# Kernel optimization log

Measured on AMD Instinct MI355X. Metric: run time of the kernel, lower is better.

## Reference

```python
import jax, jax.numpy as jnp
import numpy as np

INPUT_SIZE = 84 * 84 * 4  # 28224
FEATURE_SIZE = 1500
BATCH = 256

def setup_inputs() -> dict:
    key = jax.random.key(0)
    k_x, k_we, k_wd = jax.random.split(key, 3)
    scale_e = 1.0 / np.sqrt(INPUT_SIZE)
    scale_d = 1.0 / np.sqrt(FEATURE_SIZE)
    return {
        "x": jax.random.normal(k_x, (BATCH, INPUT_SIZE), dtype=jnp.float32),
        "W_enc": jax.random.normal(k_we, (FEATURE_SIZE, INPUT_SIZE), dtype=jnp.float32) * scale_e,
        "b_enc": jnp.zeros((FEATURE_SIZE,), dtype=jnp.float32),
        "W_dec": jax.random.normal(k_wd, (INPUT_SIZE, FEATURE_SIZE), dtype=jnp.float32) * scale_d,
        "b_dec": jnp.zeros((INPUT_SIZE,), dtype=jnp.float32),
    }

def reference(x, W_enc, b_enc, W_dec, b_dec):
    # Encoder: y_enc = sigmoid(x @ W_enc^T + b_enc), shape [B, F]
    y_enc = jax.nn.sigmoid(jnp.einsum('bi,fi->bf', x, W_enc) + b_enc)
    # Contractive (Jacobian Frobenius norm) term, closed form:
    # d y_enc[b,i] / d x[b,:] = y*(1-y) * W_enc[i,:]
    # jac_reg = sum_{b,i} (y*(1-y))^2 * ||W_enc[i,:]||^2
    s2 = jnp.square(y_enc * (1.0 - y_enc))          # [B, F]
    row_norm2 = jnp.sum(jnp.square(W_enc), axis=1)  # [F]
    jac_reg = jnp.sum(s2 * row_norm2)               # scalar
    # Decoder
    y_out = jax.nn.sigmoid(jnp.einsum('bf,if->bi', y_enc, W_dec) + b_dec)
    return y_out, jac_reg
```

## Files before the change

### kernel.cpp

```cpp
#include <hip/hip_runtime.h>
#include <hip/hip_bf16.h>


#define BATCH 256
#define IN    28224
#define FEAT  1500
#define FPAD  1536
#define KPAD  1504
#define ENC_S 21

typedef __attribute__((ext_vector_type(8))) short short8;
typedef __attribute__((ext_vector_type(4))) float f32x4;

__device__ __forceinline__ unsigned pack2(float lo, float hi) {
    unsigned a = __float_as_uint(lo) + 0x8000u;
    unsigned b = __float_as_uint(hi) + 0x8000u;
    return __builtin_amdgcn_perm(b, a, 0x07060302);
}
__device__ __forceinline__ unsigned short f2bf(float f) {
    unsigned u = __float_as_uint(f);
    return (unsigned short)((u + 0x7FFFu + ((u >> 16) & 1u)) >> 16);
}

__device__ __forceinline__ void async16(const unsigned short* g, unsigned short* l) {
    __builtin_amdgcn_global_load_lds(
        (const __attribute__((address_space(1))) unsigned int*)g,
        (__attribute__((address_space(3))) unsigned int*)l,
        16, 0, 0);
}


__global__ __launch_bounds__(256) void cvt_x(const float* __restrict__ x,
                                             unsigned short* __restrict__ xbf) {
    int idx = blockIdx.x * 256 + threadIdx.x;
    float4 v = ((const float4*)x)[idx];
    ((uint2*)xbf)[idx] = make_uint2(pack2(v.x, v.y), pack2(v.z, v.w));
}

__global__ __launch_bounds__(256) void wcvt_enc(const float* __restrict__ We,
                                                unsigned short* __restrict__ Webf,
                                                float* __restrict__ rn2) {
    const int row = blockIdx.y;
    const int t = threadIdx.x;
    const float4* src = (const float4*)(We + (long)row * IN) + blockIdx.x * 1008;
    uint2* dst = (uint2*)(Webf + (long)row * IN) + blockIdx.x * 1008;
    float sq = 0.f;
#pragma unroll
    for (int j = 0; j < 4; ++j) {
        int i = j * 256 + t;
        if (i < 1008) {
            float4 v = src[i];
            dst[i] = make_uint2(pack2(v.x, v.y), pack2(v.z, v.w));
            sq += v.x*v.x + v.y*v.y + v.z*v.z + v.w*v.w;
        }
    }
#pragma unroll
    for (int off = 32; off > 0; off >>= 1) sq += __shfl_down(sq, off);
    __shared__ float red[4];
    if ((t & 63) == 0) red[t >> 6] = sq;
    __syncthreads();
    if (t == 0) atomicAdd(&rn2[row], red[0] + red[1] + red[2] + red[3]);
}

__global__ __launch_bounds__(256) void wcvt_dec(const float* __restrict__ Wd,
                                                unsigned short* __restrict__ Wdbf) {
    int i = blockIdx.x * 256 + threadIdx.x;
    if (i >= 10584000) return;
    unsigned row = (unsigned)i / 375u;
    unsigned c   = (unsigned)i - row * 375u;
    float4 v = ((const float4*)Wd)[i];
    uint2* dst = (uint2*)Wdbf + (long)row * 376 + c;
    *dst = make_uint2(pack2(v.x, v.y), pack2(v.z, v.w));
    if (c == 374) dst[1] = make_uint2(0u, 0u);
}


__global__ __launch_bounds__(256) void enc_gemm_f(const unsigned short* __restrict__ xbf,
                                                  const unsigned short* __restrict__ Webf,
                                                  float* __restrict__ part) {
    __shared__ unsigned short As[128 * 32];
    __shared__ unsigned short Bs[64 * 32];

    const int m0 = (blockIdx.x & 1) * 128;
    const int n0 = (blockIdx.x >> 1) * 64;
    const int kb = blockIdx.y * 1344;
    const int t    = threadIdx.x;
    const int lane = t & 63;
    const int w    = t >> 6;
    const int l15  = lane & 15;
    const int quad = lane >> 4;
    const int wm   = w & 1;
    const int wn   = w >> 1;

    const unsigned short* ga0 = xbf + (long)(m0 + w * 32 + (lane >> 2)) * IN + kb + (lane & 3) * 8;
    const unsigned short* ga1 = ga0 + (long)16 * IN;
    const unsigned short* gb  = Webf + (long)(n0 + w * 16 + (lane >> 2)) * IN + kb + (lane & 3) * 8;
    unsigned short* la0 = As + (w * 32) * 32;
    unsigned short* la1 = As + (w * 32 + 16) * 32;
    unsigned short* lb  = Bs + (w * 16) * 32;

    f32x4 acc[4][2];
#pragma unroll
    for (int mt = 0; mt < 4; ++mt)
#pragma unroll
        for (int nt = 0; nt < 2; ++nt) { f32x4 z = {0.f,0.f,0.f,0.f}; acc[mt][nt] = z; }

    for (int k = 0; k < 1344; k += 32) {
        __syncthreads();
        async16(ga0 + k, la0);
        async16(ga1 + k, la1);
        async16(gb  + k, lb);
        __syncthreads();

        short8 a[4], b[2];
#pragma unroll
        for (int mt = 0; mt < 4; ++mt)
            a[mt] = *(const short8*)(As + (wm * 64 + mt * 16 + l15) * 32 + quad * 8);
#pragma unroll
        for (int nt = 0; nt < 2; ++nt)
            b[nt] = *(const short8*)(Bs + (wn * 32 + nt * 16 + l15) * 32 + quad * 8);
#pragma unroll
        for (int mt = 0; mt < 4; ++mt)
#pragma unroll
            for (int nt = 0; nt < 2; ++nt)
                acc[mt][nt] = __builtin_amdgcn_mfma_f32_16x16x32_bf16(a[mt], b[nt], acc[mt][nt], 0, 0, 0);
    }

    float* ps = part + (long)blockIdx.y * (BATCH * FPAD);
#pragma unroll
    for (int nt = 0; nt < 2; ++nt) {
        const int col = n0 + wn * 32 + nt * 16 + l15;
#pragma unroll
        for (int mt = 0; mt < 4; ++mt) {
            const int row = m0 + wm * 64 + mt * 16 + quad * 4;
#pragma unroll
            for (int r = 0; r < 4; ++r)
                ps[(long)(row + r) * FPAD + col] = acc[mt][nt][r];
        }
    }
}

__global__ __launch_bounds__(256) void act_jac_f(const float* __restrict__ part,
                                                 const float* __restrict__ be,
                                                 const float* __restrict__ rn2,
                                                 unsigned short* __restrict__ yenc,
                                                 float* __restrict__ jac) {
    const int b = blockIdx.y;
    const int f = blockIdx.x * 256 + threadIdx.x;
    float local = 0.0f;
    unsigned short h = 0;
    if (f < FEAT) {
        float p = be[f];
#pragma unroll 3
        for (int s = 0; s < ENC_S; ++s)
            p += part[(long)(s * BATCH + b) * FPAD + f];
        float y = 1.0f / (1.0f + __expf(-p));
        h = f2bf(y);
        float sg = y * (1.0f - y);
        local = sg * sg * rn2[f];
    }
    if (f < KPAD) yenc[b * KPAD + f] = h;

    float v = local;
#pragma unroll
    for (int off = 32; off > 0; off >>= 1) v += __shfl_down(v, off);
    __shared__ float red[4];
    if ((threadIdx.x & 63) == 0) red[threadIdx.x >> 6] = v;
    __syncthreads();
    if (threadIdx.x == 0) atomicAdd(jac, red[0] + red[1] + red[2] + red[3]);
}

__global__ __launch_bounds__(256) void dec_gemm_f(const unsigned short* __restrict__ yenc,
                                                  const unsigned short* __restrict__ Wdbf,
                                                  const float* __restrict__ bd,
                                                  float* __restrict__ out) {
    __shared__ unsigned short As[128 * 32];
    __shared__ unsigned short Bs[64 * 32];

    const int m0 = (blockIdx.x & 1) * 128;
    const int n0 = (blockIdx.x >> 1) * 64;
    const int t    = threadIdx.x;
    const int lane = t & 63;
    const int w    = t >> 6;
    const int l15  = lane & 15;
    const int quad = lane >> 4;
    const int wm   = w & 1;
    const int wn   = w >> 1;

    const unsigned short* ga0 = yenc + (long)(m0 + w * 32 + (lane >> 2)) * KPAD + (lane & 3) * 8;
    const unsigned short* ga1 = ga0 + (long)16 * KPAD;
    const unsigned short* gb  = Wdbf + (long)(n0 + w * 16 + (lane >> 2)) * KPAD + (lane & 3) * 8;
    unsigned short* la0 = As + (w * 32) * 32;
    unsigned short* la1 = As + (w * 32 + 16) * 32;
    unsigned short* lb  = Bs + (w * 16) * 32;

    f32x4 acc[4][2];
#pragma unroll
    for (int mt = 0; mt < 4; ++mt)
#pragma unroll
        for (int nt = 0; nt < 2; ++nt) { f32x4 z = {0.f,0.f,0.f,0.f}; acc[mt][nt] = z; }

    for (int k = 0; k < KPAD; k += 32) {
        __syncthreads();
        async16(ga0 + k, la0);
        async16(ga1 + k, la1);
        async16(gb  + k, lb);
        __syncthreads();

        short8 a[4], b[2];
#pragma unroll
        for (int mt = 0; mt < 4; ++mt)
            a[mt] = *(const short8*)(As + (wm * 64 + mt * 16 + l15) * 32 + quad * 8);
#pragma unroll
        for (int nt = 0; nt < 2; ++nt)
            b[nt] = *(const short8*)(Bs + (wn * 32 + nt * 16 + l15) * 32 + quad * 8);
#pragma unroll
        for (int mt = 0; mt < 4; ++mt)
#pragma unroll
            for (int nt = 0; nt < 2; ++nt)
                acc[mt][nt] = __builtin_amdgcn_mfma_f32_16x16x32_bf16(a[mt], b[nt], acc[mt][nt], 0, 0, 0);
    }

#pragma unroll
    for (int nt = 0; nt < 2; ++nt) {
        const int col = n0 + wn * 32 + nt * 16 + l15;
        const float bias = bd[col];
#pragma unroll
        for (int mt = 0; mt < 4; ++mt) {
            const int row = m0 + wm * 64 + mt * 16 + quad * 4;
#pragma unroll
            for (int r = 0; r < 4; ++r) {
                float v = acc[mt][nt][r] + bias;
                out[(long)(row + r) * IN + col] = 1.0f / (1.0f + __expf(-v));
            }
        }
    }
}

#define LDA 40

__global__ __launch_bounds__(256) void enc_gemm(const unsigned short* __restrict__ xbf,
                                                const float* __restrict__ We,
                                                float* __restrict__ preact,
                                                float* __restrict__ rn2) {
    __shared__ unsigned short As[256 * LDA];
    __shared__ unsigned short Bs[64 * LDA];
    const int n0 = blockIdx.x * 64;
    const int kb = blockIdx.y * 672;
    const int t = threadIdx.x, lane = t & 63, w = t >> 6, l15 = lane & 15, quad = lane >> 4;
    const unsigned short* asrc = xbf + (long)(t >> 2) * IN + (t & 3) * 8 + kb;
    unsigned short* adst = As + (t >> 2) * LDA + (t & 3) * 8;
    const int brow = t >> 3, bc4 = t & 7;
    const int f0 = n0 + brow, f1 = f0 + 32;
    const float* bsrc0 = We + (long)(f0 < FEAT ? f0 : FEAT - 1) * IN + bc4 * 4 + kb;
    const float* bsrc1 = We + (long)(f1 < FEAT ? f1 : FEAT - 1) * IN + bc4 * 4 + kb;
    unsigned short* bdst0 = Bs + brow * LDA + bc4 * 4;
    unsigned short* bdst1 = bdst0 + 32 * LDA;
    float rsq0 = 0.f, rsq1 = 0.f;
    f32x4 acc[4][4];
#pragma unroll
    for (int mt = 0; mt < 4; ++mt)
#pragma unroll
        for (int nt = 0; nt < 4; ++nt) { f32x4 z = {0.f,0.f,0.f,0.f}; acc[mt][nt] = z; }
    for (int k = 0; k < 672; k += 32) {
        short8 av[4];
#pragma unroll
        for (int j = 0; j < 4; ++j) av[j] = *(const short8*)(asrc + (long)64 * j * IN + k);
        const float4 bv0 = *(const float4*)(bsrc0 + k);
        const float4 bv1 = *(const float4*)(bsrc1 + k);
        __syncthreads();
#pragma unroll
        for (int j = 0; j < 4; ++j) *(short8*)(adst + 64 * j * LDA) = av[j];
        *(uint2*)bdst0 = make_uint2(pack2(bv0.x, bv0.y), pack2(bv0.z, bv0.w));
        *(uint2*)bdst1 = make_uint2(pack2(bv1.x, bv1.y), pack2(bv1.z, bv1.w));
        rsq0 += bv0.x*bv0.x + bv0.y*bv0.y + bv0.z*bv0.z + bv0.w*bv0.w;
        rsq1 += bv1.x*bv1.x + bv1.y*bv1.y + bv1.z*bv1.z + bv1.w*bv1.w;
        __syncthreads();
        short8 a[4], b[4];
#pragma unroll
        for (int mt = 0; mt < 4; ++mt) a[mt] = *(const short8*)(As + (w * 64 + mt * 16 + l15) * LDA + quad * 8);
#pragma unroll
        for (int nt = 0; nt < 4; ++nt) b[nt] = *(const short8*)(Bs + (nt * 16 + l15) * LDA + quad * 8);
#pragma unroll
        for (int mt = 0; mt < 4; ++mt)
#pragma unroll
            for (int nt = 0; nt < 4; ++nt)
                acc[mt][nt] = __builtin_amdgcn_mfma_f32_16x16x32_bf16(a[mt], b[nt], acc[mt][nt], 0, 0, 0);
    }
#pragma unroll
    for (int nt = 0; nt < 4; ++nt) {
        const int col = n0 + nt * 16 + l15;
        if (col < FEAT) {
#pragma unroll
            for (int mt = 0; mt < 4; ++mt) {
                float* p = preact + (long)(w * 64 + mt * 16 + quad * 4) * FEAT + col;
#pragma unroll
                for (int r = 0; r < 4; ++r) atomicAdd(p + (long)r * FEAT, acc[mt][nt][r]);
            }
        }
    }
    {
        float v0 = rsq0, v1 = rsq1;
#pragma unroll
        for (int off = 1; off < 8; off <<= 1) { v0 += __shfl_xor(v0, off); v1 += __shfl_xor(v1, off); }
        if ((lane & 7) == 0) {
            if (f0 < FEAT) atomicAdd(&rn2[f0], v0);
            if (f1 < FEAT) atomicAdd(&rn2[f1], v1);
        }
    }
}

__global__ __launch_bounds__(256) void act_jac(const float* __restrict__ preact,
                                               const float* __restrict__ be,
                                               const float* __restrict__ rn2,
                                               unsigned short* __restrict__ yenc,
                                               float* __restrict__ jac) {
    const int b = blockIdx.y;
    const int f = blockIdx.x * 256 + threadIdx.x;
    float local = 0.0f;
    unsigned short h = 0;
    if (f < FEAT) {
        float p = preact[b * FEAT + f] + be[f];
        float y = 1.0f / (1.0f + __expf(-p));
        h = f2bf(y);
        float s = y * (1.0f - y);
        local = s * s * rn2[f];
    }
    yenc[b * FPAD + f] = h;
    float v = local;
#pragma unroll
    for (int off = 32; off > 0; off >>= 1) v += __shfl_down(v, off);
    __shared__ float red[4];
    if ((threadIdx.x & 63) == 0) red[threadIdx.x >> 6] = v;
    __syncthreads();
    if (threadIdx.x == 0) atomicAdd(jac, red[0] + red[1] + red[2] + red[3]);
}

__global__ __launch_bounds__(256) void dec_gemm(const unsigned short* __restrict__ yenc,
                                                const float* __restrict__ Wd,
                                                const float* __restrict__ bd,
                                                float* __restrict__ out) {
    __shared__ unsigned short As[128 * LDA];
    __shared__ unsigned short Bs[64 * LDA];
    const int m0 = (blockIdx.x & 1) * 128;
    const int n0 = (blockIdx.x >> 1) * 64;
    const int t = threadIdx.x, lane = t & 63, w = t >> 6, l15 = lane & 15, quad = lane >> 4;
    const int mrow = (w >> 1) * 64, ncol = (w & 1) * 32;
    const unsigned short* asrc = yenc + (long)(m0 + (t >> 2)) * FPAD + (t & 3) * 8;
    unsigned short* adst = As + (t >> 2) * LDA + (t & 3) * 8;
    const float* bsrc = Wd + (long)(n0 + (t >> 3)) * FEAT + (t & 7) * 4;
    unsigned short* bdst = Bs + (t >> 3) * LDA + (t & 7) * 4;
    f32x4 acc[4][2];
#pragma unroll
    for (int mt = 0; mt < 4; ++mt)
#pragma unroll
        for (int nt = 0; nt < 2; ++nt) { f32x4 z = {0.f,0.f,0.f,0.f}; acc[mt][nt] = z; }
    for (int k = 0; k < 1504; k += 32) {
        short8 av[2];
#pragma unroll
        for (int j = 0; j < 2; ++j) av[j] = *(const short8*)(asrc + (long)64 * j * FPAD + k);
        float4 bv0, bv1;
        if (k < 1472) {
            bv0 = *(const float4*)(bsrc + k);
            bv1 = *(const float4*)(bsrc + (long)32 * FEAT + k);
        } else {
            if ((t & 7) == 7) { bv0 = make_float4(0,0,0,0); bv1 = bv0; }
            else {
                bv0 = *(const float4*)(bsrc + k);
                bv1 = *(const float4*)(bsrc + (long)32 * FEAT + k);
            }
        }
        __syncthreads();
#pragma unroll
        for (int j = 0; j < 2; ++j) *(short8*)(adst + 64 * j * LDA) = av[j];
        *(uint2*)bdst = make_uint2(pack2(bv0.x, bv0.y), pack2(bv0.z, bv0.w));
        *(uint2*)(bdst + 32 * LDA) = make_uint2(pack2(bv1.x, bv1.y), pack2(bv1.z, bv1.w));
        __syncthreads();
        short8 a[4], b[2];
#pragma unroll
        for (int mt = 0; mt < 4; ++mt) a[mt] = *(const short8*)(As + (mrow + mt * 16 + l15) * LDA + quad * 8);
#pragma unroll
        for (int nt = 0; nt < 2; ++nt) b[nt] = *(const short8*)(Bs + (ncol + nt * 16 + l15) * LDA + quad * 8);
#pragma unroll
        for (int mt = 0; mt < 4; ++mt)
#pragma unroll
            for (int nt = 0; nt < 2; ++nt)
                acc[mt][nt] = __builtin_amdgcn_mfma_f32_16x16x32_bf16(a[mt], b[nt], acc[mt][nt], 0, 0, 0);
    }
#pragma unroll
    for (int nt = 0; nt < 2; ++nt) {
        const int col = n0 + ncol + nt * 16 + l15;
        const float bias = bd[col];
#pragma unroll
        for (int mt = 0; mt < 4; ++mt) {
            const int row = m0 + mrow + mt * 16 + quad * 4;
#pragma unroll
            for (int r = 0; r < 4; ++r) {
                float v = acc[mt][nt][r] + bias;
                out[(long)(row + r) * IN + col] = 1.0f / (1.0f + __expf(-v));
            }
        }
    }
}

extern "C" void kernel_launch(void* const* d_in, const int* in_sizes, int n_in,
                              void* d_out, int out_size, void* d_ws, size_t ws_size,
                              hipStream_t stream) {
    const float* x  = (const float*)d_in[0];
    const float* We = (const float*)d_in[1];
    const float* be = (const float*)d_in[2];
    const float* Wd = (const float*)d_in[3];
    const float* bd = (const float*)d_in[4];
    float* out = (float*)d_out;
    char* ws = (char*)d_ws;

    if (ws_size >= 219858944ull) {
        unsigned short* Webf = (unsigned short*)ws;
        unsigned short* Wdbf = (unsigned short*)(ws + 86704128);
        unsigned short* xbf  = (unsigned short*)(ws + 171601920);
        unsigned short* yenc = (unsigned short*)(ws + 186052608);
        float* part          = (float*)(ws + 186822656);
        float* rn2           = (float*)(ws + 219852800);

        hipMemsetAsync(ws + 84672000, 0, 2032128, stream);
        hipMemsetAsync(rn2, 0, 6144, stream);
        hipMemsetAsync(out + 7225344, 0, 4, stream);

        cvt_x<<<7056, 256, 0, stream>>>(x, xbf);
        wcvt_enc<<<dim3(7, 1500), 256, 0, stream>>>(We, Webf, rn2);
        wcvt_dec<<<41344, 256, 0, stream>>>(Wd, Wdbf);
        enc_gemm_f<<<dim3(48, ENC_S), 256, 0, stream>>>(xbf, Webf, part);
        act_jac_f<<<dim3(6, 256), 256, 0, stream>>>(part, be, rn2, yenc, out + 7225344);
        dec_gemm_f<<<882, 256, 0, stream>>>(yenc, Wdbf, bd, out);
    } else {
        float* preact        = (float*)ws;
        float* rn2           = (float*)(ws + 1536000);
        unsigned short* yenc = (unsigned short*)(ws + 1542144);
        unsigned short* xbf  = (unsigned short*)(ws + 2328576);

        hipMemsetAsync(ws, 0, 1542144, stream);
        hipMemsetAsync(out + 7225344, 0, 4, stream);

        cvt_x<<<7056, 256, 0, stream>>>(x, xbf);
        enc_gemm<<<dim3(24, 42), 256, 0, stream>>>(xbf, We, preact, rn2);
        act_jac<<<dim3(6, 256), 256, 0, stream>>>(preact, be, rn2, yenc, out + 7225344);
        dec_gemm<<<882, 256, 0, stream>>>(yenc, Wd, bd, out);
    }
}
```

Before: 546.7 us.

## Fuse fp32-to-bf16 weight conversion into encoder and decoder GEMM tile loads

Removes the separate weight conversion kernels and the bf16 weight copies in workspace. The encoder and decoder GEMMs now read fp32 weights directly, convert them in registers while staging into shared memory, and prefetch the next tile. Row norms are computed inside the encoder. Tiles grow to 256x64 so each block covers the whole batch and every weight tile is read once, which halves the block count. The cost is a larger per-block register and LDS footprint and fewer blocks, so each GEMM has less parallelism.

```diff
diff --git a/kernel.cpp b/kernel.cpp
--- a/kernel.cpp
+++ b/kernel.cpp
@@ -37,107 +37,91 @@
     ((uint2*)xbf)[idx] = make_uint2(pack2(v.x, v.y), pack2(v.z, v.w));
 }
 
-__global__ __launch_bounds__(256) void wcvt_enc(const float* __restrict__ We,
-                                                unsigned short* __restrict__ Webf,
-                                                float* __restrict__ rn2) {
-    const int row = blockIdx.y;
-    const int t = threadIdx.x;
-    const float4* src = (const float4*)(We + (long)row * IN) + blockIdx.x * 1008;
-    uint2* dst = (uint2*)(Webf + (long)row * IN) + blockIdx.x * 1008;
-    float sq = 0.f;
-#pragma unroll
-    for (int j = 0; j < 4; ++j) {
-        int i = j * 256 + t;
-        if (i < 1008) {
-            float4 v = src[i];
-            dst[i] = make_uint2(pack2(v.x, v.y), pack2(v.z, v.w));
-            sq += v.x*v.x + v.y*v.y + v.z*v.z + v.w*v.w;
-        }
-    }
-#pragma unroll
-    for (int off = 32; off > 0; off >>= 1) sq += __shfl_down(sq, off);
-    __shared__ float red[4];
-    if ((t & 63) == 0) red[t >> 6] = sq;
-    __syncthreads();
-    if (t == 0) atomicAdd(&rn2[row], red[0] + red[1] + red[2] + red[3]);
-}
-
-__global__ __launch_bounds__(256) void wcvt_dec(const float* __restrict__ Wd,
-                                                unsigned short* __restrict__ Wdbf) {
-    int i = blockIdx.x * 256 + threadIdx.x;
-    if (i >= 10584000) return;
-    unsigned row = (unsigned)i / 375u;
-    unsigned c   = (unsigned)i - row * 375u;
-    float4 v = ((const float4*)Wd)[i];
-    uint2* dst = (uint2*)Wdbf + (long)row * 376 + c;
-    *dst = make_uint2(pack2(v.x, v.y), pack2(v.z, v.w));
-    if (c == 374) dst[1] = make_uint2(0u, 0u);
-}
-
-
-__global__ __launch_bounds__(256) void enc_gemm_f(const unsigned short* __restrict__ xbf,
-                                                  const unsigned short* __restrict__ Webf,
-                                                  float* __restrict__ part) {
-    __shared__ unsigned short As[128 * 32];
+
+__global__ __launch_bounds__(256) void enc_fused(const unsigned short* __restrict__ xbf,
+                                                 const float* __restrict__ We,
+                                                 float* __restrict__ part,
+                                                 float* __restrict__ rn2) {
+    __shared__ unsigned short As[256 * 32];
     __shared__ unsigned short Bs[64 * 32];
 
-    const int m0 = (blockIdx.x & 1) * 128;
-    const int n0 = (blockIdx.x >> 1) * 64;
+    const int n0 = blockIdx.x * 64;
     const int kb = blockIdx.y * 1344;
     const int t    = threadIdx.x;
     const int lane = t & 63;
     const int w    = t >> 6;
     const int l15  = lane & 15;
     const int quad = lane >> 4;
-    const int wm   = w & 1;
-    const int wn   = w >> 1;
-
-    const unsigned short* ga0 = xbf + (long)(m0 + w * 32 + (lane >> 2)) * IN + kb + (lane & 3) * 8;
-    const unsigned short* ga1 = ga0 + (long)16 * IN;
-    const unsigned short* gb  = Webf + (long)(n0 + w * 16 + (lane >> 2)) * IN + kb + (lane & 3) * 8;
-    unsigned short* la0 = As + (w * 32) * 32;
-    unsigned short* la1 = As + (w * 32 + 16) * 32;
-    unsigned short* lb  = Bs + (w * 16) * 32;
-
-    f32x4 acc[4][2];
+
+    const unsigned short* ga = xbf + (long)(w * 64 + (lane >> 2)) * IN + kb + (lane & 3) * 8;
+    unsigned short* la = As + (w * 64) * 32;
+
+    const int br = t >> 2;
+    const int bf_ = n0 + br;
+    const bool bvalid = bf_ < FEAT;
+    const float* bsrc = We + (long)(bvalid ? bf_ : FEAT - 1) * IN + kb + (t & 3) * 8;
+    unsigned short* bdst = Bs + br * 32 + (t & 3) * 8;
+
+    float rsq = 0.f;
+    f32x4 acc[4][4];
 #pragma unroll
     for (int mt = 0; mt < 4; ++mt)
 #pragma unroll
-        for (int nt = 0; nt < 2; ++nt) { f32x4 z = {0.f,0.f,0.f,0.f}; acc[mt][nt] = z; }
+        for (int nt = 0; nt < 4; ++nt) { f32x4 z = {0.f,0.f,0.f,0.f}; acc[mt][nt] = z; }
+
+    float4 v0 = *(const float4*)(bsrc);
+    float4 v1 = *(const float4*)(bsrc + 4);
 
     for (int k = 0; k < 1344; k += 32) {
         __syncthreads();
-        async16(ga0 + k, la0);
-        async16(ga1 + k, la1);
-        async16(gb  + k, lb);
-        __syncthreads();
-
-        short8 a[4], b[2];
-#pragma unroll
-        for (int mt = 0; mt < 4; ++mt)
-            a[mt] = *(const short8*)(As + (wm * 64 + mt * 16 + l15) * 32 + quad * 8);
-#pragma unroll
-        for (int nt = 0; nt < 2; ++nt)
-            b[nt] = *(const short8*)(Bs + (wn * 32 + nt * 16 + l15) * 32 + quad * 8);
-#pragma unroll
-        for (int mt = 0; mt < 4; ++mt)
-#pragma unroll
-            for (int nt = 0; nt < 2; ++nt)
+        async16(ga + k,            la);
+        async16(ga + 16 * IN + k,  la + 16 * 32);
+        async16(ga + 32 * IN + k,  la + 32 * 32);
+        async16(ga + 48 * IN + k,  la + 48 * 32);
+        uint2 p0 = make_uint2(pack2(v0.x, v0.y), pack2(v0.z, v0.w));
+        uint2 p1 = make_uint2(pack2(v1.x, v1.y), pack2(v1.z, v1.w));
+        if (!bvalid) { p0 = make_uint2(0u, 0u); p1 = make_uint2(0u, 0u); }
+        *(uint2*)bdst       = p0;
+        *(uint2*)(bdst + 4) = p1;
+        rsq += v0.x*v0.x + v0.y*v0.y + v0.z*v0.z + v0.w*v0.w
+             + v1.x*v1.x + v1.y*v1.y + v1.z*v1.z + v1.w*v1.w;
+        const int kn = k + 32;
+        if (kn < 1344) {
+            v0 = *(const float4*)(bsrc + kn);
+            v1 = *(const float4*)(bsrc + kn + 4);
+        }
+        __syncthreads();
+
+        short8 a[4], b[4];
+#pragma unroll
+        for (int mt = 0; mt < 4; ++mt)
+            a[mt] = *(const short8*)(As + (w * 64 + mt * 16 + l15) * 32 + quad * 8);
+#pragma unroll
+        for (int nt = 0; nt < 4; ++nt)
+            b[nt] = *(const short8*)(Bs + (nt * 16 + l15) * 32 + quad * 8);
+#pragma unroll
+        for (int mt = 0; mt < 4; ++mt)
+#pragma unroll
+            for (int nt = 0; nt < 4; ++nt)
                 acc[mt][nt] = __builtin_amdgcn_mfma_f32_16x16x32_bf16(a[mt], b[nt], acc[mt][nt], 0, 0, 0);
     }
 
     float* ps = part + (long)blockIdx.y * (BATCH * FPAD);
 #pragma unroll
-    for (int nt = 0; nt < 2; ++nt) {
-        const int col = n0 + wn * 32 + nt * 16 + l15;
+    for (int nt = 0; nt < 4; ++nt) {
+        const int col = n0 + nt * 16 + l15;
 #pragma unroll
         for (int mt = 0; mt < 4; ++mt) {
-            const int row = m0 + wm * 64 + mt * 16 + quad * 4;
+            const int row = w * 64 + mt * 16 + quad * 4;
 #pragma unroll
             for (int r = 0; r < 4; ++r)
                 ps[(long)(row + r) * FPAD + col] = acc[mt][nt][r];
         }
     }
+
+    rsq += __shfl_xor(rsq, 1);
+    rsq += __shfl_xor(rsq, 2);
+    if ((lane & 3) == 0 && bvalid) atomicAdd(&rn2[bf_], rsq);
 }
 
 __global__ __launch_bounds__(256) void act_jac_f(const float* __restrict__ part,
@@ -170,64 +154,75 @@
     if (threadIdx.x == 0) atomicAdd(jac, red[0] + red[1] + red[2] + red[3]);
 }
 
-__global__ __launch_bounds__(256) void dec_gemm_f(const unsigned short* __restrict__ yenc,
-                                                  const unsigned short* __restrict__ Wdbf,
-                                                  const float* __restrict__ bd,
-                                                  float* __restrict__ out) {
-    __shared__ unsigned short As[128 * 32];
+__global__ __launch_bounds__(256) void dec_fused(const unsigned short* __restrict__ yenc,
+                                                 const float* __restrict__ Wd,
+                                                 const float* __restrict__ bd,
+                                                 float* __restrict__ out) {
+    __shared__ unsigned short As[256 * 32];
     __shared__ unsigned short Bs[64 * 32];
 
-    const int m0 = (blockIdx.x & 1) * 128;
-    const int n0 = (blockIdx.x >> 1) * 64;
+    const int n0 = blockIdx.x * 64;
     const int t    = threadIdx.x;
     const int lane = t & 63;
     const int w    = t >> 6;
     const int l15  = lane & 15;
     const int quad = lane >> 4;
-    const int wm   = w & 1;
-    const int wn   = w >> 1;
-
-    const unsigned short* ga0 = yenc + (long)(m0 + w * 32 + (lane >> 2)) * KPAD + (lane & 3) * 8;
-    const unsigned short* ga1 = ga0 + (long)16 * KPAD;
-    const unsigned short* gb  = Wdbf + (long)(n0 + w * 16 + (lane >> 2)) * KPAD + (lane & 3) * 8;
-    unsigned short* la0 = As + (w * 32) * 32;
-    unsigned short* la1 = As + (w * 32 + 16) * 32;
-    unsigned short* lb  = Bs + (w * 16) * 32;
-
-    f32x4 acc[4][2];
+
+    const unsigned short* ga = yenc + (long)(w * 64 + (lane >> 2)) * KPAD + (lane & 3) * 8;
+    unsigned short* la = As + (w * 64) * 32;
+
+    const int br = t >> 2;
+    const int bn = n0 + br;
+    const float* bsrc = Wd + (long)bn * FEAT + (t & 3) * 8;
+    unsigned short* bdst = Bs + br * 32 + (t & 3) * 8;
+
+    f32x4 acc[4][4];
 #pragma unroll
     for (int mt = 0; mt < 4; ++mt)
 #pragma unroll
-        for (int nt = 0; nt < 2; ++nt) { f32x4 z = {0.f,0.f,0.f,0.f}; acc[mt][nt] = z; }
+        for (int nt = 0; nt < 4; ++nt) { f32x4 z = {0.f,0.f,0.f,0.f}; acc[mt][nt] = z; }
+
+    float4 v0 = *(const float4*)(bsrc);
+    float4 v1 = *(const float4*)(bsrc + 4);
 
     for (int k = 0; k < KPAD; k += 32) {
         __syncthreads();
-        async16(ga0 + k, la0);
-        async16(ga1 + k, la1);
-        async16(gb  + k, lb);
-        __syncthreads();
-
-        short8 a[4], b[2];
-#pragma unroll
-        for (int mt = 0; mt < 4; ++mt)
-            a[mt] = *(const short8*)(As + (wm * 64 + mt * 16 + l15) * 32 + quad * 8);
-#pragma unroll
-        for (int nt = 0; nt < 2; ++nt)
-            b[nt] = *(const short8*)(Bs + (wn * 32 + nt * 16 + l15) * 32 + quad * 8);
-#pragma unroll
-        for (int mt = 0; mt < 4; ++mt)
-#pragma unroll
-            for (int nt = 0; nt < 2; ++nt)
+        async16(ga + k,              la);
+        async16(ga + 16 * KPAD + k,  la + 16 * 32);
+        async16(ga + 32 * KPAD + k,  la + 32 * 32);
+        async16(ga + 48 * KPAD + k,  la + 48 * 32);
+        *(uint2*)bdst       = make_uint2(pack2(v0.x, v0.y), pack2(v0.z, v0.w));
+        *(uint2*)(bdst + 4) = make_uint2(pack2(v1.x, v1.y), pack2(v1.z, v1.w));
+        const int kn = k + 32;
+        if (kn < KPAD) {
+            v0 = *(const float4*)(bsrc + kn);
+            const int cc = kn + (t & 3) * 8 + 4;
+            if (cc + 3 < FEAT) v1 = *(const float4*)(bsrc + kn + 4);
+            else               v1 = make_float4(0.f, 0.f, 0.f, 0.f);
+        }
+        __syncthreads();
+
+        short8 a[4], b[4];
+#pragma unroll
+        for (int mt = 0; mt < 4; ++mt)
+            a[mt] = *(const short8*)(As + (w * 64 + mt * 16 + l15) * 32 + quad * 8);
+#pragma unroll
+        for (int nt = 0; nt < 4; ++nt)
+            b[nt] = *(const short8*)(Bs + (nt * 16 + l15) * 32 + quad * 8);
+#pragma unroll
+        for (int mt = 0; mt < 4; ++mt)
+#pragma unroll
+            for (int nt = 0; nt < 4; ++nt)
                 acc[mt][nt] = __builtin_amdgcn_mfma_f32_16x16x32_bf16(a[mt], b[nt], acc[mt][nt], 0, 0, 0);
     }
 
 #pragma unroll
-    for (int nt = 0; nt < 2; ++nt) {
-        const int col = n0 + wn * 32 + nt * 16 + l15;
+    for (int nt = 0; nt < 4; ++nt) {
+        const int col = n0 + nt * 16 + l15;
         const float bias = bd[col];
 #pragma unroll
         for (int mt = 0; mt < 4; ++mt) {
-            const int row = m0 + wm * 64 + mt * 16 + quad * 4;
+            const int row = w * 64 + mt * 16 + quad * 4;
 #pragma unroll
             for (int r = 0; r < 4; ++r) {
                 float v = acc[mt][nt][r] + bias;
@@ -414,24 +409,19 @@
     float* out = (float*)d_out;
     char* ws = (char*)d_ws;
 
-    if (ws_size >= 219858944ull) {
-        unsigned short* Webf = (unsigned short*)ws;
-        unsigned short* Wdbf = (unsigned short*)(ws + 86704128);
-        unsigned short* xbf  = (unsigned short*)(ws + 171601920);
-        unsigned short* yenc = (unsigned short*)(ws + 186052608);
-        float* part          = (float*)(ws + 186822656);
-        float* rn2           = (float*)(ws + 219852800);
-
-        hipMemsetAsync(ws + 84672000, 0, 2032128, stream);
+    if (ws_size >= 48257024ull) {
+        unsigned short* xbf  = (unsigned short*)ws;
+        unsigned short* yenc = (unsigned short*)(ws + 14450688);
+        float* part          = (float*)(ws + 15220736);
+        float* rn2           = (float*)(ws + 48250880);
+
         hipMemsetAsync(rn2, 0, 6144, stream);
         hipMemsetAsync(out + 7225344, 0, 4, stream);
 
         cvt_x<<<7056, 256, 0, stream>>>(x, xbf);
-        wcvt_enc<<<dim3(7, 1500), 256, 0, stream>>>(We, Webf, rn2);
-        wcvt_dec<<<41344, 256, 0, stream>>>(Wd, Wdbf);
-        enc_gemm_f<<<dim3(48, ENC_S), 256, 0, stream>>>(xbf, Webf, part);
+        enc_fused<<<dim3(24, ENC_S), 256, 0, stream>>>(xbf, We, part, rn2);
         act_jac_f<<<dim3(6, 256), 256, 0, stream>>>(part, be, rn2, yenc, out + 7225344);
-        dec_gemm_f<<<882, 256, 0, stream>>>(yenc, Wdbf, bd, out);
+        dec_fused<<<441, 256, 0, stream>>>(yenc, Wd, bd, out);
     } else {
         float* preact        = (float*)ws;
         float* rn2           = (float*)(ws + 1536000);
```

New measurement: 462.8 us. -15.3%, faster.
